# Performance work log

Hardware: AMD Instinct MI355X
Metric: run time of the kernel (lower is better)

## Reference

```python
import jax, jax.numpy as jnp
import numpy as np

# dims
B, S, E, H, W = 32, 256, 512, 512, 512   # batch, max_sentence_length, word_emb, rnn_units, weight_size
ENC = 2 * H                               # bidirectional encoder hidden
V = 50000                                 # vocab


def setup_inputs() -> dict:
    key = jax.random.key(0)
    ks = jax.random.split(key, 16)
    n = jax.random.normal
    return {
        "word_ids": jax.random.randint(ks[0], (B, S), 0, V),
        "encoder_outputs": n(ks[1], (B, S, ENC), jnp.float32),
        "encoder_hn": n(ks[2], (B, H), jnp.float32),          # initial decoder cell state
        "emb": n(ks[3], (V, E), jnp.float32) * 0.02,          # WordFeature embedding table
        "chunk_emb": n(ks[4], (S, W), jnp.float32) * 0.02,    # chunk_length_embedding
        "W1": n(ks[5], (ENC, W), jnp.float32) / np.sqrt(ENC),
        "W2": n(ks[6], (E, W), jnp.float32) / np.sqrt(E),
        "W3": n(ks[7], (E, W), jnp.float32) / np.sqrt(E),
        "W4": n(ks[8], (H, W), jnp.float32) / np.sqrt(H),
        "vt1": n(ks[9], (W,), jnp.float32) / np.sqrt(W),
        "vt2": n(ks[10], (W,), jnp.float32) / np.sqrt(W),
        "Wx": n(ks[11], (E, 4 * H), jnp.float32) / np.sqrt(E),  # decoder LSTM cell
        "Wh": n(ks[12], (H, 4 * H), jnp.float32) / np.sqrt(H),
        "bias": jnp.zeros((4 * H,), jnp.float32),
    }


def reference(word_ids, encoder_outputs, encoder_hn, emb, chunk_emb,
              W1, W2, W3, W4, vt1, vt2, Wx, Wh, bias):
    Ss = word_ids.shape[1]
    Hh = encoder_hn.shape[1]
    inp = emb[word_ids]                                   # [B,S,E] word features
    b1 = jnp.einsum('bse,ew->bsw', encoder_outputs, W1)   # W1(encoder_output), hoisted
    b2 = jnp.einsum('bse,ew->bsw', inp, W2)               # W2(single_input), hoisted
    pos = jnp.arange(Ss)

    def decode_one(inp_b, b1_b, b2_b, c0):
        def step(carry, _):
            last_bond, bond, h, c, out_vec = carry
            done = bond >= Ss
            # decoder input: mean of current segment inp[last_bond:bond] (zeros at step 0)
            m = ((pos >= last_bond) & (pos < bond)).astype(inp_b.dtype)  # [S]
            x = (m @ inp_b) / jnp.maximum(m.sum(), 1.0)                  # [E]
            # LSTM cell (stand-in for decoder.pointer_forward)
            gates = x @ Wx + h @ Wh + bias                               # [4H]
            i_g, f_g, g_g, o_g = jnp.split(gates, 4)
            c_n = jax.nn.sigmoid(f_g) * c + jax.nn.sigmoid(i_g) * jnp.tanh(g_g)
            h_n = jax.nn.sigmoid(o_g) * jnp.tanh(c_n)
            h2 = jnp.where(done, h, h_n)
            c2 = jnp.where(done, c, c_n)
            bidx = jnp.minimum(bond, Ss - 1)
            # pointer attention over positions >= bond
            blend = jnp.tanh(b1_b + b2_b + inp_b[bidx] @ W3 + h2 @ W4)   # [S,W]
            seg_len = jnp.clip(bond - last_bond, 0, Ss - 1)
            scores = blend @ vt1 + chunk_emb[seg_len] @ vt2              # [S]
            scores = jnp.where(pos >= bidx, scores, -1e30)
            # log_softmax is monotonic -> argmax of scores == argmax of log-probs
            idx = jnp.argmax(scores)                                     # absolute = max_index + bond
            new_bond = jnp.where(idx > bond, idx, bond + 1)              # force progress
            widx = jnp.minimum(new_bond, Ss - 1)
            val = jnp.where((~done) & (new_bond < Ss), 1.0, out_vec[widx])
            out_new = out_vec.at[widx].set(val)
            last2 = jnp.where(done, last_bond, bond)
            bond2 = jnp.where(done, bond, new_bond)
            return (last2, bond2, h2, c2, out_new), None

        init = (jnp.int32(0), jnp.int32(0),
                jnp.zeros((Hh,), inp_b.dtype), c0,
                jnp.zeros((Ss,), inp_b.dtype))
        (_, _, _, _, out_vec), _ = jax.lax.scan(step, init, None, length=Ss)
        return out_vec

    outs = jax.vmap(decode_one)(inp, b1, b2, encoder_hn)   # [B,S]
    return outs.T                                          # [S,B] == torch.stack(output_list, 1)
```

## Files before the change

### kernel.cpp

```cpp
#include <hip/hip_runtime.h>
#include <math.h>

#define Bn   32
#define Sn   256
#define En   512
#define Hn   512
#define Wn   512
#define ENCn 1024
#define G4   2048
#define KTOT 1536
#define NC   8
#define WPC  32

#define OFF_BSUM  0L
#define OFF_U3    4194304L
#define OFF_PE    8388608L
#define OFF_WB    12599296L
#define OFF_W4B   14696448L
#define OFF_GATES 14958592L
#define OFF_H     15089664L
#define OFF_C     15106048L
#define OFF_SPART 15138816L
#define OFF_STATE 15204352L


__device__ __forceinline__ float aload(const float* p) {
    return __hip_atomic_load(p, __ATOMIC_RELAXED, __HIP_MEMORY_SCOPE_AGENT);
}
__device__ __forceinline__ void astore(float* p, float v) {
    __hip_atomic_store(p, v, __ATOMIC_RELAXED, __HIP_MEMORY_SCOPE_AGENT);
}
__device__ __forceinline__ int aiload(const int* p) {
    return __hip_atomic_load(p, __ATOMIC_RELAXED, __HIP_MEMORY_SCOPE_AGENT);
}
__device__ __forceinline__ void aistore(int* p, int v) {
    __hip_atomic_store(p, v, __ATOMIC_RELAXED, __HIP_MEMORY_SCOPE_AGENT);
}

__global__ void init_kernel(const float* __restrict__ hn0, float* __restrict__ h,
                            float* __restrict__ c, int* __restrict__ state)
{
    int i = blockIdx.x * blockDim.x + threadIdx.x;
    if (i < Bn * Hn) { h[i] = 0.0f; c[i] = hn0[i]; }
    if (i < 8192) state[i] = (i == 64) ? Bn : 0;
}

__global__ void wtrans_kernel(const float* __restrict__ Wx, const float* __restrict__ Wh,
                              const float* __restrict__ W4, float* __restrict__ WB,
                              float* __restrict__ W4B)
{
    int idx = blockIdx.x * 256 + threadIdx.x;
    if (idx < 2097152) {
        const int cc = idx & 3, l = (idx >> 2) & 63, kq = (idx >> 8) & 255, cb = idx >> 16;
        const int k = 4 * kq + cc, j = cb * 64 + l;
        WB[idx] = (k < 512) ? Wx[(long)k * G4 + j] : Wh[(long)(k - 512) * G4 + j];
    }
    if (idx < 262144) {
        const int cc = idx & 3, l = (idx >> 2) & 63, kq = (idx >> 8) & 127, cb = idx >> 15;
        const int k = 4 * kq + cc, j = cb * 64 + l;
        W4B[idx] = W4[(long)k * Wn + j];
    }
}

__global__ void pe1_kernel(const int* __restrict__ wid, const float* __restrict__ emb,
                           float* __restrict__ pb)
{
    const int b = blockIdx.x, blk = blockIdx.y;
    __shared__ int wids[16];
    if (threadIdx.x < 16) wids[threadIdx.x] = wid[b * Sn + blk * 16 + threadIdx.x];
    __syncthreads();
    float a0 = 0.f, a1 = 0.f;
    for (int s = 0; s < 16; ++s) {
        const float* r = emb + (long)wids[s] * En;
        a0 += r[threadIdx.x]; a1 += r[threadIdx.x + 256];
    }
    pb[((long)b * 16 + blk) * En + threadIdx.x] = a0;
    pb[((long)b * 16 + blk) * En + threadIdx.x + 256] = a1;
}

__global__ void pe2_kernel(const int* __restrict__ wid, const float* __restrict__ emb,
                           const float* __restrict__ pb, float* __restrict__ pe)
{
    const int b = blockIdx.x, blk = blockIdx.y;
    __shared__ int wids[16];
    if (threadIdx.x < 16) wids[threadIdx.x] = wid[b * Sn + blk * 16 + threadIdx.x];
    __syncthreads();
    float a0 = 0.f, a1 = 0.f;
    for (int j = 0; j < blk; ++j) {
        a0 += pb[((long)b * 16 + j) * En + threadIdx.x];
        a1 += pb[((long)b * 16 + j) * En + threadIdx.x + 256];
    }
    float* base = pe + (long)b * 257 * En;
    if (blk == 0) { base[threadIdx.x] = 0.f; base[threadIdx.x + 256] = 0.f; }
    for (int s = 0; s < 16; ++s) {
        const float* r = emb + (long)wids[s] * En;
        a0 += r[threadIdx.x]; a1 += r[threadIdx.x + 256];
        float* o = base + (long)(blk * 16 + s + 1) * En;
        o[threadIdx.x] = a0; o[threadIdx.x + 256] = a1;
    }
}

__global__ __launch_bounds__(256) void bsum_gemm(
    const float* __restrict__ enc, const int* __restrict__ wid,
    const float* __restrict__ emb, const float* __restrict__ W1,
    const float* __restrict__ W2, float* __restrict__ bsum)
{
    __shared__ float As[16][68];
    __shared__ float Bs[16][68];
    const int tid  = threadIdx.x;
    const int row0 = blockIdx.y * 64;
    const int col0 = blockIdx.x * 64;
    const int tm0  = (tid & 15) * 4;
    const int tn0  = (tid >> 4) * 4;
    const int la_r = tid >> 2;
    const int la_k = (tid & 3) * 4;
    const int lb_k = tid >> 4;
    const int lb_n = (tid & 15) * 4;

    float acc[4][4];
#pragma unroll
    for (int i = 0; i < 4; i++)
#pragma unroll
        for (int j = 0; j < 4; j++) acc[i][j] = 0.0f;

    for (int k0 = 0; k0 < KTOT; k0 += 16) {
        const int gr = row0 + la_r;
        float4 av;
        if (k0 < ENCn) {
            av = *(const float4*)&enc[(long)gr * ENCn + k0 + la_k];
        } else {
            const int wv = wid[gr];
            av = *(const float4*)&emb[(long)wv * En + (k0 - ENCn) + la_k];
        }
        As[la_k + 0][la_r] = av.x;
        As[la_k + 1][la_r] = av.y;
        As[la_k + 2][la_r] = av.z;
        As[la_k + 3][la_r] = av.w;
        float4 bv;
        if (k0 < ENCn) bv = *(const float4*)&W1[(long)(k0 + lb_k) * Wn + col0 + lb_n];
        else           bv = *(const float4*)&W2[(long)(k0 - ENCn + lb_k) * Wn + col0 + lb_n];
        *(float4*)&Bs[lb_k][lb_n] = bv;
        __syncthreads();
#pragma unroll
        for (int kk = 0; kk < 16; kk++) {
            float4 a = *(const float4*)&As[kk][tm0];
            float4 b = *(const float4*)&Bs[kk][tn0];
            acc[0][0] += a.x * b.x; acc[0][1] += a.x * b.y; acc[0][2] += a.x * b.z; acc[0][3] += a.x * b.w;
            acc[1][0] += a.y * b.x; acc[1][1] += a.y * b.y; acc[1][2] += a.y * b.z; acc[1][3] += a.y * b.w;
            acc[2][0] += a.z * b.x; acc[2][1] += a.z * b.y; acc[2][2] += a.z * b.z; acc[2][3] += a.z * b.w;
            acc[3][0] += a.w * b.x; acc[3][1] += a.w * b.y; acc[3][2] += a.w * b.z; acc[3][3] += a.w * b.w;
        }
        __syncthreads();
    }
#pragma unroll
    for (int i = 0; i < 4; i++) {
        float4 o = make_float4(acc[i][0], acc[i][1], acc[i][2], acc[i][3]);
        *(float4*)&bsum[(long)(row0 + tm0 + i) * Wn + col0 + tn0] = o;
    }
}

__global__ __launch_bounds__(256) void u3_gemm(
    const int* __restrict__ wid, const float* __restrict__ emb,
    const float* __restrict__ W3, float* __restrict__ u3)
{
    __shared__ float As[16][68];
    __shared__ float Bs[16][68];
    const int tid  = threadIdx.x;
    const int row0 = blockIdx.y * 64;
    const int col0 = blockIdx.x * 64;
    const int tm0  = (tid & 15) * 4;
    const int tn0  = (tid >> 4) * 4;
    const int la_r = tid >> 2;
    const int la_k = (tid & 3) * 4;
    const int lb_k = tid >> 4;
    const int lb_n = (tid & 15) * 4;

    float acc[4][4];
#pragma unroll
    for (int i = 0; i < 4; i++)
#pragma unroll
        for (int j = 0; j < 4; j++) acc[i][j] = 0.0f;

    for (int k0 = 0; k0 < 512; k0 += 16) {
        const int gr = row0 + la_r;
        const int wv = wid[gr];
        float4 av = *(const float4*)&emb[(long)wv * En + k0 + la_k];
        As[la_k + 0][la_r] = av.x;
        As[la_k + 1][la_r] = av.y;
        As[la_k + 2][la_r] = av.z;
        As[la_k + 3][la_r] = av.w;
        *(float4*)&Bs[lb_k][lb_n] = *(const float4*)&W3[(long)(k0 + lb_k) * Wn + col0 + lb_n];
        __syncthreads();
#pragma unroll
        for (int kk = 0; kk < 16; kk++) {
            float4 a = *(const float4*)&As[kk][tm0];
            float4 b = *(const float4*)&Bs[kk][tn0];
            acc[0][0] += a.x * b.x; acc[0][1] += a.x * b.y; acc[0][2] += a.x * b.z; acc[0][3] += a.x * b.w;
            acc[1][0] += a.y * b.x; acc[1][1] += a.y * b.y; acc[1][2] += a.y * b.z; acc[1][3] += a.y * b.w;
            acc[2][0] += a.z * b.x; acc[2][1] += a.z * b.y; acc[2][2] += a.z * b.z; acc[2][3] += a.z * b.w;
            acc[3][0] += a.w * b.x; acc[3][1] += a.w * b.y; acc[3][2] += a.w * b.z; acc[3][3] += a.w * b.w;
        }
        __syncthreads();
    }
#pragma unroll
    for (int i = 0; i < 4; i++) {
        float4 o = make_float4(acc[i][0], acc[i][1], acc[i][2], acc[i][3]);
        *(float4*)&u3[(long)(row0 + tm0 + i) * Wn + col0 + tn0] = o;
    }
}

__device__ __forceinline__ int gbar(int* st, const int* nact, int wg, int round)
{
    __shared__ int s_done;
    __syncthreads();
    if (threadIdx.x == 0) {
        const int c = wg >> 5;
        int* lc = st + 4096 + 256 * c;
        int* lr = lc + 64;
        int flag = 0;
        bool wait = true;
        int a = __hip_atomic_fetch_add(lc, 1, __ATOMIC_RELAXED, __HIP_MEMORY_SCOPE_AGENT);
        if (a == round * WPC - 1) {
            int g = __hip_atomic_fetch_add(st + 80, 1, __ATOMIC_RELAXED, __HIP_MEMORY_SCOPE_AGENT);
            if (g == round * NC - 1) {
                const int d = (aiload(nact) == 0) ? (1 << 30) : 0;
                flag = round | d;
                for (int k = 0; k < NC; ++k)
                    aistore(st + 4096 + 256 * k + 64, flag);
                wait = false;
            }
        }
        if (wait) {
            for (;;) {
                flag = aiload(lr);
                if ((flag & 0x3FFFFFFF) >= round) break;
                __builtin_amdgcn_s_sleep(1);
            }
        }
        s_done = (flag >> 30) & 1;
    }
    __syncthreads();
    return s_done;
}

__global__ __launch_bounds__(256) void decode_kernel(
    const float* __restrict__ bias, const float* __restrict__ vt1,
    const float* __restrict__ bsum, const float* __restrict__ u3,
    const float* __restrict__ pe,   const float* __restrict__ WB,
    const float* __restrict__ W4B,  float* __restrict__ gpart,
    float* __restrict__ hbuf, float* __restrict__ cbuf,
    float* __restrict__ spart,
    int* __restrict__ state, float* __restrict__ out)
{
    __shared__ __align__(16) float wlds[32768];
    __shared__ __align__(16) float sx[4096];
    __shared__ __align__(16) float sred[2048];
    __shared__ float s_svt[64];
    __shared__ float s_wv[4];
    __shared__ int   s_wi[4];
    __shared__ int   s_last;
    __shared__ int   s_bd[8], s_ls[8];

    const int wg   = blockIdx.x;
    const int tid  = threadIdx.x;
    const int lane = tid & 63;
    const int wv   = tid >> 6;

    int* bond = state;
    int* last = state + 32;
    int* nact = state + 64;

    const int cb1 = wg & 31;
    const int kh  = (wg >> 5) & 1;
    const int bg  = wg >> 6;
    const int b2  = wg >> 3;
    const int cb2 = wg & 7;
    const float4* W4B4 = (const float4*)W4B;
    float4* wlds4 = (float4*)wlds;
    float4* sx4   = (float4*)sx;

    {
        const float4* src = (const float4*)WB + ((long)cb1 * 256 + kh * 128) * 64;
        for (int i = tid; i < 8192; i += 256) wlds4[i] = src[i];
    }
    if (tid < 64) s_svt[tid] = vt1[cb2 * 64 + tid];

    int myround = 0;

    for (int step = 0; step < Sn; ++step) {
        const float* cold = cbuf + (step & 1) * (Bn * Hn);
        float*       cnew = cbuf + ((step + 1) & 1) * (Bn * Hn);

        if (tid < 8) {
            s_bd[tid] = aiload(&bond[bg * 8 + tid]);
            s_ls[tid] = aiload(&last[bg * 8 + tid]);
        }
        __syncthreads();
        for (int idx = tid; idx < 4096; idx += 256) {
            const int bq = idx >> 9, k = idx & 511;
            const int b  = bg * 8 + bq;
            float v;
            if (kh == 0) {
                const int bd = s_bd[bq], ls = s_ls[bq];
                const float inv = 1.0f / (float)max(bd - ls, 1);
                v = (pe[((long)b * 257 + bd) * En + k] - pe[((long)b * 257 + ls) * En + k]) * inv;
            } else {
                v = aload(&hbuf[b * Hn + k]);
            }
            sx[idx] = v;
        }
        __syncthreads();
        {
            float acc[8] = {0.f,0.f,0.f,0.f,0.f,0.f,0.f,0.f};
            const float4* wl = wlds4 + (wv * 32) * 64 + lane;
#pragma unroll 8
            for (int kq = 0; kq < 32; ++kq) {
                const float4 w = wl[kq * 64];
                const int kb = wv * 32 + kq;
#pragma unroll
                for (int bq = 0; bq < 8; ++bq) {
                    const float4 xv = sx4[bq * 128 + kb];
                    acc[bq] += w.x * xv.x + w.y * xv.y + w.z * xv.z + w.w * xv.w;
                }
            }
#pragma unroll
            for (int bq = 0; bq < 8; ++bq)
                sred[wv * 512 + bq * 64 + lane] = acc[bq];
        }
        __syncthreads();
#pragma unroll
        for (int o = tid; o < 512; o += 256) {
            const int bq = o >> 6;
            if (s_bd[bq] < Sn) {
                const float s = sred[o] + sred[512 + o] + sred[1024 + o] + sred[1536 + o];
                astore(&gpart[((long)(kh * Bn) + bg * 8 + bq) * G4 + cb1 * 64 + (o & 63)], s);
            }
        }
        gbar(state, nact, wg, 2 * step + 1);

        const int bd = aiload(&bond[b2]);
        if (bd < Sn) {
            ++myround;
            const float* gp0 = gpart + (long)b2 * G4;
            const float* gp1 = gpart + (long)(Bn + b2) * G4;
            for (int j = tid; j < Hn; j += 256) {
                const float ig = aload(&gp0[j])        + aload(&gp1[j])        + bias[j];
                const float fg = aload(&gp0[512 + j])  + aload(&gp1[512 + j])  + bias[512 + j];
                const float gg = aload(&gp0[1024 + j]) + aload(&gp1[1024 + j]) + bias[1024 + j];
                const float og = aload(&gp0[1536 + j]) + aload(&gp1[1536 + j]) + bias[1536 + j];
                const float co = aload(&cold[b2 * Hn + j]);
                const float sf  = 1.f / (1.f + expf(-fg));
                const float sig = 1.f / (1.f + expf(-ig));
                const float so  = 1.f / (1.f + expf(-og));
                const float cn  = sf * co + sig * tanhf(gg);
                const float h2  = so * tanhf(cn);
                sx[j] = h2;
                if (cb2 == 0) { astore(&hbuf[b2 * Hn + j], h2); astore(&cnew[b2 * Hn + j], cn); }
            }
            __syncthreads();
            {
                float acc = 0.f;
                const float4* wrow = W4B4 + ((long)cb2 * 128 + wv * 32) * 64 + lane;
#pragma unroll 8
                for (int kq = 0; kq < 32; ++kq) {
                    const float4 w  = wrow[(long)kq * 64];
                    const float4 xv = sx4[wv * 32 + kq];
                    acc += w.x * xv.x + w.y * xv.y + w.z * xv.z + w.w * xv.w;
                }
                sx[512 + wv * 64 + lane] = acc;
            }
            __syncthreads();
            if (tid < 64) {
                const float* u3row = u3 + ((long)b2 * Sn + bd) * Wn + cb2 * 64;
                sx[768 + tid] = sx[512 + tid] + sx[576 + tid] + sx[640 + tid]
                              + sx[704 + tid] + u3row[tid];
            }
            __syncthreads();
            if (tid >= bd) {
                const float* row = bsum + ((long)b2 * Sn + tid) * Wn + cb2 * 64;
                float a = 0.f;
#pragma unroll 8
                for (int i = 0; i < 64; ++i)
                    a += tanhf(row[i] + sx[768 + i]) * s_svt[i];
                astore(&spart[((long)b2 * 8 + cb2) * 256 + tid], a);
            }
            __syncthreads();
            if (tid == 0) {
                int o = __hip_atomic_fetch_add(state + 256 + 64 * b2, 1,
                                               __ATOMIC_RELAXED, __HIP_MEMORY_SCOPE_AGENT);
                s_last = (o == myround * 8 - 1);
            }
            __syncthreads();
            if (s_last) {
                float v = -3.402823e38f; int vi = Sn;
                if (tid >= bd) {
                    const float* sp = spart + (long)b2 * 8 * 256 + tid;
                    float s = 0.f;
#pragma unroll
                    for (int k = 0; k < 8; ++k) s += aload(&sp[k * 256]);
                    v = s; vi = tid;
                }
#pragma unroll
                for (int off = 32; off; off >>= 1) {
                    const float v2 = __shfl_xor(v, off, 64);
                    const int   i2 = __shfl_xor(vi, off, 64);
                    if (v2 > v || (v2 == v && i2 < vi)) { v = v2; vi = i2; }
                }
                if (lane == 0) { s_wv[wv] = v; s_wi[wv] = vi; }
                __syncthreads();
                if (tid == 0) {
                    float bv = s_wv[0]; int bi = s_wi[0];
#pragma unroll
                    for (int k = 1; k < 4; ++k)
                        if (s_wv[k] > bv || (s_wv[k] == bv && s_wi[k] < bi)) { bv = s_wv[k]; bi = s_wi[k]; }
                    const int nb2 = (bi > bd) ? bi : bd + 1;
                    if (nb2 < Sn) out[nb2 * Bn + b2] = 1.0f;
                    else __hip_atomic_fetch_add(nact, -1, __ATOMIC_RELAXED, __HIP_MEMORY_SCOPE_AGENT);
                    aistore(&last[b2], bd);
                    aistore(&bond[b2], nb2);
                }
            }
        }
        if (gbar(state, nact, wg, 2 * step + 2)) break;
    }
}

extern "C" void kernel_launch(void* const* d_in, const int* in_sizes, int n_in,
                              void* d_out, int out_size, void* d_ws, size_t ws_size,
                              hipStream_t stream)
{
    const int*   wid  = (const int*)d_in[0];
    const float* enc  = (const float*)d_in[1];
    const float* hn0  = (const float*)d_in[2];
    const float* emb  = (const float*)d_in[3];
    const float* W1   = (const float*)d_in[5];
    const float* W2   = (const float*)d_in[6];
    const float* W3   = (const float*)d_in[7];
    const float* W4   = (const float*)d_in[8];
    const float* vt1  = (const float*)d_in[9];
    const float* Wx   = (const float*)d_in[11];
    const float* Wh   = (const float*)d_in[12];
    const float* bias = (const float*)d_in[13];

    float* ws    = (float*)d_ws;
    float* bsum  = ws + OFF_BSUM;
    float* u3    = ws + OFF_U3;
    float* pb    = ws + OFF_U3;
    float* pe    = ws + OFF_PE;
    float* WB    = ws + OFF_WB;
    float* W4B   = ws + OFF_W4B;
    float* gpart = ws + OFF_GATES;
    float* h     = ws + OFF_H;
    float* c     = ws + OFF_C;
    float* spart = ws + OFF_SPART;
    int*   state = (int*)(ws + OFF_STATE);
    float* out   = (float*)d_out;

    hipMemsetAsync(d_out, 0, (size_t)Sn * Bn * sizeof(float), stream);
    hipLaunchKernelGGL(init_kernel, dim3(64), dim3(256), 0, stream, hn0, h, c, state);
    hipLaunchKernelGGL(wtrans_kernel, dim3(8192), dim3(256), 0, stream, Wx, Wh, W4, WB, W4B);
    hipLaunchKernelGGL(pe1_kernel, dim3(32, 16), dim3(256), 0, stream, wid, emb, pb);
    hipLaunchKernelGGL(pe2_kernel, dim3(32, 16), dim3(256), 0, stream, wid, emb, pb, pe);
    hipLaunchKernelGGL(u3_gemm, dim3(8, 128), dim3(256), 0, stream, wid, emb, W3, u3);
    hipLaunchKernelGGL(bsum_gemm, dim3(8, 128), dim3(256), 0, stream, enc, wid, emb, W1, W2, bsum);

    void* args[] = { (void*)&bias, (void*)&vt1, (void*)&bsum, (void*)&u3, (void*)&pe,
                     (void*)&WB, (void*)&W4B, (void*)&gpart, (void*)&h, (void*)&c,
                     (void*)&spart, (void*)&state, (void*)&out };
    hipLaunchCooperativeKernel((void*)decode_kernel, dim3(256), dim3(256), args, 0, stream);
}
```

Baseline: 923.5 us.

## Replace global grid barriers with per-batch counters and packed state flags

```diff
diff --git a/kernel.cpp b/kernel.cpp
--- a/kernel.cpp
+++ b/kernel.cpp
@@ -9,8 +9,6 @@
 #define ENCn 1024
 #define G4   2048
 #define KTOT 1536
-#define NC   8
-#define WPC  32
 
 #define OFF_BSUM  0L
 #define OFF_U3    4194304L
@@ -33,7 +31,10 @@
 __device__ __forceinline__ int aiload(const int* p) {
     return __hip_atomic_load(p, __ATOMIC_RELAXED, __HIP_MEMORY_SCOPE_AGENT);
 }
-__device__ __forceinline__ void aistore(int* p, int v) {
+__device__ __forceinline__ unsigned long long aload64(const unsigned long long* p) {
+    return __hip_atomic_load(p, __ATOMIC_RELAXED, __HIP_MEMORY_SCOPE_AGENT);
+}
+__device__ __forceinline__ void astore64(unsigned long long* p, unsigned long long v) {
     __hip_atomic_store(p, v, __ATOMIC_RELAXED, __HIP_MEMORY_SCOPE_AGENT);
 }
 
@@ -42,7 +43,7 @@
 {
     int i = blockIdx.x * blockDim.x + threadIdx.x;
     if (i < Bn * Hn) { h[i] = 0.0f; c[i] = hn0[i]; }
-    if (i < 8192) state[i] = (i == 64) ? Bn : 0;
+    if (i < 8192) state[i] = (i == 1024) ? Bn : 0;
 }
 
 __global__ void wtrans_kernel(const float* __restrict__ Wx, const float* __restrict__ Wh,
@@ -209,40 +210,6 @@
     }
 }
 
-__device__ __forceinline__ int gbar(int* st, const int* nact, int wg, int round)
-{
-    __shared__ int s_done;
-    __syncthreads();
-    if (threadIdx.x == 0) {
-        const int c = wg >> 5;
-        int* lc = st + 4096 + 256 * c;
-        int* lr = lc + 64;
-        int flag = 0;
-        bool wait = true;
-        int a = __hip_atomic_fetch_add(lc, 1, __ATOMIC_RELAXED, __HIP_MEMORY_SCOPE_AGENT);
-        if (a == round * WPC - 1) {
-            int g = __hip_atomic_fetch_add(st + 80, 1, __ATOMIC_RELAXED, __HIP_MEMORY_SCOPE_AGENT);
-            if (g == round * NC - 1) {
-                const int d = (aiload(nact) == 0) ? (1 << 30) : 0;
-                flag = round | d;
-                for (int k = 0; k < NC; ++k)
-                    aistore(st + 4096 + 256 * k + 64, flag);
-                wait = false;
-            }
-        }
-        if (wait) {
-            for (;;) {
-                flag = aiload(lr);
-                if ((flag & 0x3FFFFFFF) >= round) break;
-                __builtin_amdgcn_s_sleep(1);
-            }
-        }
-        s_done = (flag >> 30) & 1;
-    }
-    __syncthreads();
-    return s_done;
-}
-
 __global__ __launch_bounds__(256) void decode_kernel(
     const float* __restrict__ bias, const float* __restrict__ vt1,
     const float* __restrict__ bsum, const float* __restrict__ u3,
@@ -260,21 +227,24 @@
     __shared__ int   s_wi[4];
     __shared__ int   s_last;
     __shared__ int   s_bd[8], s_ls[8];
+    __shared__ int   s_exit;
 
     const int wg   = blockIdx.x;
     const int tid  = threadIdx.x;
     const int lane = tid & 63;
     const int wv   = tid >> 6;
 
-    int* bond = state;
-    int* last = state + 32;
-    int* nact = state + 64;
+    int* gcnt = state;
+    int* scnt = state + 512;
+    int* nact = state + 1024;
+    unsigned long long* s64b = (unsigned long long*)(state + 1536);
 
     const int cb1 = wg & 31;
     const int kh  = (wg >> 5) & 1;
     const int bg  = wg >> 6;
     const int b2  = wg >> 3;
     const int cb2 = wg & 7;
+    const int bq2 = (wg >> 3) & 7;
     const float4* W4B4 = (const float4*)W4B;
     float4* wlds4 = (float4*)wlds;
     float4* sx4   = (float4*)sx;
@@ -285,62 +255,94 @@
     }
     if (tid < 64) s_svt[tid] = vt1[cb2 * 64 + tid];
 
-    int myround = 0;
-
-    for (int step = 0; step < Sn; ++step) {
-        const float* cold = cbuf + (step & 1) * (Bn * Hn);
-        float*       cnew = cbuf + ((step + 1) & 1) * (Bn * Hn);
-
-        if (tid < 8) {
-            s_bd[tid] = aiload(&bond[bg * 8 + tid]);
-            s_ls[tid] = aiload(&last[bg * 8 + tid]);
+    int a_b = 0;
+
+    for (int t = 1; t <= Sn; ++t) {
+        if (tid < 64) {
+            const bool isb = tid < 8;
+            const unsigned long long* sp = s64b + 8 * (bg * 8 + (tid & 7));
+            for (;;) {
+                unsigned long long pk = isb ? aload64(sp) : 0ULL;
+                const int ep = (int)(pk & 0xffffu);
+                const int bd = (int)((pk >> 16) & 0xffffu);
+                const bool ok = !isb || (ep >= t - 1) || (bd >= Sn);
+                int ex = 0;
+                if (tid == 8) ex = (aiload(nact) == 0);
+                const unsigned long long bal  = __ballot(ok);
+                const unsigned long long balx = __ballot(ex != 0);
+                if (((bal & 0xffULL) == 0xffULL) || balx) {
+                    if (isb) { s_bd[tid] = bd; s_ls[tid] = (int)((pk >> 32) & 0xffffu); }
+                    if (tid == 0) s_exit = (balx != 0ULL);
+                    break;
+                }
+                __builtin_amdgcn_s_sleep(1);
+            }
         }
         __syncthreads();
-        for (int idx = tid; idx < 4096; idx += 256) {
-            const int bq = idx >> 9, k = idx & 511;
-            const int b  = bg * 8 + bq;
-            float v;
-            if (kh == 0) {
-                const int bd = s_bd[bq], ls = s_ls[bq];
-                const float inv = 1.0f / (float)max(bd - ls, 1);
-                v = (pe[((long)b * 257 + bd) * En + k] - pe[((long)b * 257 + ls) * En + k]) * inv;
-            } else {
-                v = aload(&hbuf[b * Hn + k]);
-            }
-            sx[idx] = v;
-        }
-        __syncthreads();
-        {
-            float acc[8] = {0.f,0.f,0.f,0.f,0.f,0.f,0.f,0.f};
-            const float4* wl = wlds4 + (wv * 32) * 64 + lane;
+        if (s_exit) break;
+
+        int anyact = 0;
+#pragma unroll
+        for (int q = 0; q < 8; ++q) anyact |= (s_bd[q] < Sn);
+
+        if (anyact) {
+            for (int idx = tid; idx < 4096; idx += 256) {
+                const int bq = idx >> 9, k = idx & 511;
+                const int b  = bg * 8 + bq;
+                float v = 0.f;
+                if (s_bd[bq] < Sn) {
+                    if (kh == 0) {
+                        const int bd = s_bd[bq], ls = s_ls[bq];
+                        const float inv = 1.0f / (float)max(bd - ls, 1);
+                        v = (pe[((long)b * 257 + bd) * En + k] - pe[((long)b * 257 + ls) * En + k]) * inv;
+                    } else {
+                        v = aload(&hbuf[b * Hn + k]);
+                    }
+                }
+                sx[idx] = v;
+            }
+            __syncthreads();
+            {
+                float acc[8] = {0.f,0.f,0.f,0.f,0.f,0.f,0.f,0.f};
+                const float4* wl = wlds4 + (wv * 32) * 64 + lane;
 #pragma unroll 8
-            for (int kq = 0; kq < 32; ++kq) {
-                const float4 w = wl[kq * 64];
-                const int kb = wv * 32 + kq;
-#pragma unroll
-                for (int bq = 0; bq < 8; ++bq) {
-                    const float4 xv = sx4[bq * 128 + kb];
-                    acc[bq] += w.x * xv.x + w.y * xv.y + w.z * xv.z + w.w * xv.w;
-                }
-            }
-#pragma unroll
-            for (int bq = 0; bq < 8; ++bq)
-                sred[wv * 512 + bq * 64 + lane] = acc[bq];
-        }
-        __syncthreads();
-#pragma unroll
-        for (int o = tid; o < 512; o += 256) {
-            const int bq = o >> 6;
-            if (s_bd[bq] < Sn) {
-                const float s = sred[o] + sred[512 + o] + sred[1024 + o] + sred[1536 + o];
-                astore(&gpart[((long)(kh * Bn) + bg * 8 + bq) * G4 + cb1 * 64 + (o & 63)], s);
-            }
-        }
-        gbar(state, nact, wg, 2 * step + 1);
-
-        const int bd = aiload(&bond[b2]);
+                for (int kq = 0; kq < 32; ++kq) {
+                    const float4 w = wl[kq * 64];
+                    const int kb = wv * 32 + kq;
+#pragma unroll
+                    for (int bq = 0; bq < 8; ++bq) {
+                        const float4 xv = sx4[bq * 128 + kb];
+                        acc[bq] += w.x * xv.x + w.y * xv.y + w.z * xv.z + w.w * xv.w;
+                    }
+                }
+#pragma unroll
+                for (int bq = 0; bq < 8; ++bq)
+                    sred[wv * 512 + bq * 64 + lane] = acc[bq];
+            }
+            __syncthreads();
+#pragma unroll
+            for (int o = tid; o < 512; o += 256) {
+                const int bq = o >> 6;
+                if (s_bd[bq] < Sn) {
+                    const float s = sred[o] + sred[512 + o] + sred[1024 + o] + sred[1536 + o];
+                    astore(&gpart[((long)(kh * Bn) + bg * 8 + bq) * G4 + cb1 * 64 + (o & 63)], s);
+                }
+            }
+            __syncthreads();
+        }
+        if (tid < 8)
+            __hip_atomic_fetch_add(&gcnt[16 * (bg * 8 + tid)], 1,
+                                   __ATOMIC_RELAXED, __HIP_MEMORY_SCOPE_AGENT);
+
+        const int bd = s_bd[bq2];
         if (bd < Sn) {
-            ++myround;
+            ++a_b;
+            const float* cold = cbuf + ((a_b - 1) & 1) * (Bn * Hn);
+            float*       cnew = cbuf + (a_b & 1) * (Bn * Hn);
+            if (tid == 0) {
+                while (aiload(&gcnt[16 * b2]) < 64 * t) __builtin_amdgcn_s_sleep(1);
+            }
+            __syncthreads();
             const float* gp0 = gpart + (long)b2 * G4;
             const float* gp1 = gpart + (long)(Bn + b2) * G4;
             for (int j = tid; j < Hn; j += 256) {
@@ -386,9 +388,9 @@
             }
             __syncthreads();
             if (tid == 0) {
-                int o = __hip_atomic_fetch_add(state + 256 + 64 * b2, 1,
+                int o = __hip_atomic_fetch_add(&scnt[16 * b2], 1,
                                                __ATOMIC_RELAXED, __HIP_MEMORY_SCOPE_AGENT);
-                s_last = (o == myround * 8 - 1);
+                s_last = (o == 8 * a_b - 1);
             }
             __syncthreads();
             if (s_last) {
@@ -416,12 +418,14 @@
                     const int nb2 = (bi > bd) ? bi : bd + 1;
                     if (nb2 < Sn) out[nb2 * Bn + b2] = 1.0f;
                     else __hip_atomic_fetch_add(nact, -1, __ATOMIC_RELAXED, __HIP_MEMORY_SCOPE_AGENT);
-                    aistore(&last[b2], bd);
-                    aistore(&bond[b2], nb2);
-                }
-            }
-        }
-        if (gbar(state, nact, wg, 2 * step + 2)) break;
+                    const unsigned long long pk =
+                        (unsigned long long)(unsigned)t |
+                        ((unsigned long long)(unsigned)nb2 << 16) |
+                        ((unsigned long long)(unsigned)bd  << 32);
+                    astore64(&s64b[8 * b2], pk);
+                }
+            }
+        }
     }
 }
 
```

Result: faster. 865.7 us (-6.3%).

## Precompute prefix-sum input projection and replace global barriers with per-batch flags

Applied to the files above, without the earlier changes.

```diff
diff --git a/kernel.cpp b/kernel.cpp
--- a/kernel.cpp
+++ b/kernel.cpp
@@ -9,20 +9,18 @@
 #define ENCn 1024
 #define G4   2048
 #define KTOT 1536
-#define NC   8
-#define WPC  32
 
 #define OFF_BSUM  0L
-#define OFF_U3    4194304L
-#define OFF_PE    8388608L
-#define OFF_WB    12599296L
-#define OFF_W4B   14696448L
-#define OFF_GATES 14958592L
-#define OFF_H     15089664L
-#define OFF_C     15106048L
-#define OFF_SPART 15138816L
-#define OFF_STATE 15204352L
-
+#define OFF_PWX   4194304L
+#define OFF_PE    21037056L
+#define OFF_U3    21037056L
+#define OFF_WHB   25247744L
+#define OFF_W4B   26296320L
+#define OFF_GPH   26558464L
+#define OFF_SPART 26689536L
+#define OFF_STATE 26820608L
+
+typedef unsigned long long u64t;
 
 __device__ __forceinline__ float aload(const float* p) {
     return __hip_atomic_load(p, __ATOMIC_RELAXED, __HIP_MEMORY_SCOPE_AGENT);
@@ -36,24 +34,32 @@
 __device__ __forceinline__ void aistore(int* p, int v) {
     __hip_atomic_store(p, v, __ATOMIC_RELAXED, __HIP_MEMORY_SCOPE_AGENT);
 }
-
-__global__ void init_kernel(const float* __restrict__ hn0, float* __restrict__ h,
-                            float* __restrict__ c, int* __restrict__ state)
+__device__ __forceinline__ u64t aload64(const u64t* p) {
+    return __hip_atomic_load(p, __ATOMIC_RELAXED, __HIP_MEMORY_SCOPE_AGENT);
+}
+__device__ __forceinline__ void astore64(u64t* p, u64t v) {
+    __hip_atomic_store(p, v, __ATOMIC_RELAXED, __HIP_MEMORY_SCOPE_AGENT);
+}
+__device__ __forceinline__ u64t pack2(float a, float b) {
+    return (u64t)__float_as_uint(a) | ((u64t)__float_as_uint(b) << 32);
+}
+__device__ __forceinline__ float lo32(u64t v) { return __uint_as_float((unsigned)(v & 0xffffffffu)); }
+__device__ __forceinline__ float hi32(u64t v) { return __uint_as_float((unsigned)(v >> 32)); }
+
+__global__ void init_kernel(float* __restrict__ gph, int* __restrict__ state)
 {
     int i = blockIdx.x * blockDim.x + threadIdx.x;
-    if (i < Bn * Hn) { h[i] = 0.0f; c[i] = hn0[i]; }
-    if (i < 8192) state[i] = (i == 64) ? Bn : 0;
-}
-
-__global__ void wtrans_kernel(const float* __restrict__ Wx, const float* __restrict__ Wh,
-                              const float* __restrict__ W4, float* __restrict__ WB,
-                              float* __restrict__ W4B)
+    if (i < 131072) gph[i] = 0.0f;
+    if (i < 8192) state[i] = (i < 512) ? 1 : 0;
+}
+
+__global__ void wtrans_kernel(const float* __restrict__ Wh, const float* __restrict__ W4,
+                              float* __restrict__ WhB, float* __restrict__ W4B)
 {
     int idx = blockIdx.x * 256 + threadIdx.x;
-    if (idx < 2097152) {
-        const int cc = idx & 3, l = (idx >> 2) & 63, kq = (idx >> 8) & 255, cb = idx >> 16;
-        const int k = 4 * kq + cc, j = cb * 64 + l;
-        WB[idx] = (k < 512) ? Wx[(long)k * G4 + j] : Wh[(long)(k - 512) * G4 + j];
+    if (idx < 1048576) {
+        const int c = idx & 255, k = (idx >> 8) & 511, cb = idx >> 17;
+        WhB[idx] = Wh[(long)k * G4 + cb * 256 + c];
     }
     if (idx < 262144) {
         const int cc = idx & 3, l = (idx >> 2) & 63, kq = (idx >> 8) & 127, cb = idx >> 15;
@@ -159,9 +165,8 @@
     }
 }
 
-__global__ __launch_bounds__(256) void u3_gemm(
-    const int* __restrict__ wid, const float* __restrict__ emb,
-    const float* __restrict__ W3, float* __restrict__ u3)
+__global__ __launch_bounds__(256) void swx_gemm(
+    const float* __restrict__ pe, const float* __restrict__ Wx, float* __restrict__ PWX)
 {
     __shared__ float As[16][68];
     __shared__ float Bs[16][68];
@@ -182,6 +187,58 @@
         for (int j = 0; j < 4; j++) acc[i][j] = 0.0f;
 
     for (int k0 = 0; k0 < 512; k0 += 16) {
+        int gr = row0 + la_r; if (gr > 8223) gr = 8223;
+        float4 av = *(const float4*)&pe[(long)gr * En + k0 + la_k];
+        As[la_k + 0][la_r] = av.x;
+        As[la_k + 1][la_r] = av.y;
+        As[la_k + 2][la_r] = av.z;
+        As[la_k + 3][la_r] = av.w;
+        *(float4*)&Bs[lb_k][lb_n] = *(const float4*)&Wx[(long)(k0 + lb_k) * G4 + col0 + lb_n];
+        __syncthreads();
+#pragma unroll
+        for (int kk = 0; kk < 16; kk++) {
+            float4 a = *(const float4*)&As[kk][tm0];
+            float4 b = *(const float4*)&Bs[kk][tn0];
+            acc[0][0] += a.x * b.x; acc[0][1] += a.x * b.y; acc[0][2] += a.x * b.z; acc[0][3] += a.x * b.w;
+            acc[1][0] += a.y * b.x; acc[1][1] += a.y * b.y; acc[1][2] += a.y * b.z; acc[1][3] += a.y * b.w;
+            acc[2][0] += a.z * b.x; acc[2][1] += a.z * b.y; acc[2][2] += a.z * b.z; acc[2][3] += a.z * b.w;
+            acc[3][0] += a.w * b.x; acc[3][1] += a.w * b.y; acc[3][2] += a.w * b.z; acc[3][3] += a.w * b.w;
+        }
+        __syncthreads();
+    }
+#pragma unroll
+    for (int i = 0; i < 4; i++) {
+        const int r = row0 + tm0 + i;
+        if (r < 8224) {
+            float4 o = make_float4(acc[i][0], acc[i][1], acc[i][2], acc[i][3]);
+            *(float4*)&PWX[(long)r * G4 + col0 + tn0] = o;
+        }
+    }
+}
+
+__global__ __launch_bounds__(256) void u3_gemm(
+    const int* __restrict__ wid, const float* __restrict__ emb,
+    const float* __restrict__ W3, float* __restrict__ u3)
+{
+    __shared__ float As[16][68];
+    __shared__ float Bs[16][68];
+    const int tid  = threadIdx.x;
+    const int row0 = blockIdx.y * 64;
+    const int col0 = blockIdx.x * 64;
+    const int tm0  = (tid & 15) * 4;
+    const int tn0  = (tid >> 4) * 4;
+    const int la_r = tid >> 2;
+    const int la_k = (tid & 3) * 4;
+    const int lb_k = tid >> 4;
+    const int lb_n = (tid & 15) * 4;
+
+    float acc[4][4];
+#pragma unroll
+    for (int i = 0; i < 4; i++)
+#pragma unroll
+        for (int j = 0; j < 4; j++) acc[i][j] = 0.0f;
+
+    for (int k0 = 0; k0 < 512; k0 += 16) {
         const int gr = row0 + la_r;
         const int wv = wid[gr];
         float4 av = *(const float4*)&emb[(long)wv * En + k0 + la_k];
@@ -209,219 +266,190 @@
     }
 }
 
-__device__ __forceinline__ int gbar(int* st, const int* nact, int wg, int round)
-{
-    __shared__ int s_done;
-    __syncthreads();
-    if (threadIdx.x == 0) {
-        const int c = wg >> 5;
-        int* lc = st + 4096 + 256 * c;
-        int* lr = lc + 64;
-        int flag = 0;
-        bool wait = true;
-        int a = __hip_atomic_fetch_add(lc, 1, __ATOMIC_RELAXED, __HIP_MEMORY_SCOPE_AGENT);
-        if (a == round * WPC - 1) {
-            int g = __hip_atomic_fetch_add(st + 80, 1, __ATOMIC_RELAXED, __HIP_MEMORY_SCOPE_AGENT);
-            if (g == round * NC - 1) {
-                const int d = (aiload(nact) == 0) ? (1 << 30) : 0;
-                flag = round | d;
-                for (int k = 0; k < NC; ++k)
-                    aistore(st + 4096 + 256 * k + 64, flag);
-                wait = false;
-            }
-        }
-        if (wait) {
-            for (;;) {
-                flag = aiload(lr);
-                if ((flag & 0x3FFFFFFF) >= round) break;
-                __builtin_amdgcn_s_sleep(1);
-            }
-        }
-        s_done = (flag >> 30) & 1;
-    }
-    __syncthreads();
-    return s_done;
-}
-
 __global__ __launch_bounds__(256) void decode_kernel(
     const float* __restrict__ bias, const float* __restrict__ vt1,
     const float* __restrict__ bsum, const float* __restrict__ u3,
-    const float* __restrict__ pe,   const float* __restrict__ WB,
-    const float* __restrict__ W4B,  float* __restrict__ gpart,
-    float* __restrict__ hbuf, float* __restrict__ cbuf,
-    float* __restrict__ spart,
-    int* __restrict__ state, float* __restrict__ out)
+    const float* __restrict__ PWX,  const float* __restrict__ WhB,
+    const float* __restrict__ W4B,  float* __restrict__ gphbuf,
+    float* __restrict__ spart, int* __restrict__ state,
+    const float* __restrict__ hn0, float* __restrict__ out)
 {
     __shared__ __align__(16) float wlds[32768];
-    __shared__ __align__(16) float sx[4096];
-    __shared__ __align__(16) float sred[2048];
+    __shared__ __align__(16) float pwx[2][2048];
+    __shared__ __align__(16) float hld[512];
+    __shared__ __align__(16) float cld[512];
+    __shared__ __align__(16) float sgph[4][256];
+    __shared__ __align__(16) float sred4[4][64];
+    __shared__ float qv[64];
     __shared__ float s_svt[64];
     __shared__ float s_wv[4];
     __shared__ int   s_wi[4];
-    __shared__ int   s_last;
-    __shared__ int   s_bd[8], s_ls[8];
 
     const int wg   = blockIdx.x;
     const int tid  = threadIdx.x;
     const int lane = tid & 63;
     const int wv   = tid >> 6;
-
-    int* bond = state;
-    int* last = state + 32;
-    int* nact = state + 64;
-
-    const int cb1 = wg & 31;
-    const int kh  = (wg >> 5) & 1;
-    const int bg  = wg >> 6;
-    const int b2  = wg >> 3;
-    const int cb2 = wg & 7;
+    const int b    = wg >> 3;
+    const int cb2  = wg & 7;
+
+    int* gflag = state;
+    int* sflag = state + 512;
+    u64t* gph64 = (u64t*)gphbuf;
     const float4* W4B4 = (const float4*)W4B;
     float4* wlds4 = (float4*)wlds;
-    float4* sx4   = (float4*)sx;
+    const float4* h4 = (const float4*)hld;
 
     {
-        const float4* src = (const float4*)WB + ((long)cb1 * 256 + kh * 128) * 64;
+        const float4* src = W4B4 + (long)cb2 * 8192;
         for (int i = tid; i < 8192; i += 256) wlds4[i] = src[i];
     }
     if (tid < 64) s_svt[tid] = vt1[cb2 * 64 + tid];
-
-    int myround = 0;
-
-    for (int step = 0; step < Sn; ++step) {
-        const float* cold = cbuf + (step & 1) * (Bn * Hn);
-        float*       cnew = cbuf + ((step + 1) & 1) * (Bn * Hn);
+    cld[tid]       = hn0[b * Hn + tid];
+    cld[256 + tid] = hn0[b * Hn + 256 + tid];
+    hld[tid] = 0.f; hld[256 + tid] = 0.f;
+    {
+        const float4* pr = (const float4*)(PWX + (long)b * 257 * G4);
+        float4* d = (float4*)pwx[0];
+        for (int i = tid; i < 512; i += 256) d[i] = pr[i];
+    }
+    const float2* bias2 = (const float2*)bias;
+    const float2 bi  = bias2[tid];
+    const float2 bf  = bias2[256 + tid];
+    const float2 bg_ = bias2[512 + tid];
+    const float2 bo  = bias2[768 + tid];
+    __syncthreads();
+
+    int bd = 0, ls = 0;
+
+    for (int t = 1; t <= Sn; ++t) {
+        const int cur = t & 1, prv = cur ^ 1;
 
         if (tid < 8) {
-            s_bd[tid] = aiload(&bond[bg * 8 + tid]);
-            s_ls[tid] = aiload(&last[bg * 8 + tid]);
-        }
-        __syncthreads();
-        for (int idx = tid; idx < 4096; idx += 256) {
-            const int bq = idx >> 9, k = idx & 511;
-            const int b  = bg * 8 + bq;
-            float v;
-            if (kh == 0) {
-                const int bd = s_bd[bq], ls = s_ls[bq];
-                const float inv = 1.0f / (float)max(bd - ls, 1);
-                v = (pe[((long)b * 257 + bd) * En + k] - pe[((long)b * 257 + ls) * En + k]) * inv;
-            } else {
-                v = aload(&hbuf[b * Hn + k]);
-            }
-            sx[idx] = v;
+            const int* g = gflag + 16 * b + tid;
+            while (aiload(g) < t) __builtin_amdgcn_s_sleep(1);
         }
         __syncthreads();
         {
-            float acc[8] = {0.f,0.f,0.f,0.f,0.f,0.f,0.f,0.f};
-            const float4* wl = wlds4 + (wv * 32) * 64 + lane;
+            const float4* pr = (const float4*)(PWX + ((long)b * 257 + bd) * G4);
+            float4* d = (float4*)pwx[cur];
+            for (int i = tid; i < 512; i += 256) d[i] = pr[i];
+        }
+        float u3v = 0.f;
+        if (tid < 64) u3v = aload(&u3[((long)b * Sn + bd) * Wn + cb2 * 64 + tid]);
+        const long gb = (long)cur * 32768 + (long)b * 1024;
+        const u64t g0 = aload64(&gph64[gb + tid]);
+        const u64t g1 = aload64(&gph64[gb + 256 + tid]);
+        const u64t g2 = aload64(&gph64[gb + 512 + tid]);
+        const u64t g3 = aload64(&gph64[gb + 768 + tid]);
+        __syncthreads();
+
+        {
+            const float inv = 1.0f / (float)max(bd - ls, 1);
+            const int j0 = 2 * tid, j1 = j0 + 1;
+            const float igA = (pwx[cur][j0]        - pwx[prv][j0])        * inv + lo32(g0) + bi.x;
+            const float igB = (pwx[cur][j1]        - pwx[prv][j1])        * inv + hi32(g0) + bi.y;
+            const float fgA = (pwx[cur][512 + j0]  - pwx[prv][512 + j0])  * inv + lo32(g1) + bf.x;
+            const float fgB = (pwx[cur][512 + j1]  - pwx[prv][512 + j1])  * inv + hi32(g1) + bf.y;
+            const float ggA = (pwx[cur][1024 + j0] - pwx[prv][1024 + j0]) * inv + lo32(g2) + bg_.x;
+            const float ggB = (pwx[cur][1024 + j1] - pwx[prv][1024 + j1]) * inv + hi32(g2) + bg_.y;
+            const float ogA = (pwx[cur][1536 + j0] - pwx[prv][1536 + j0]) * inv + lo32(g3) + bo.x;
+            const float ogB = (pwx[cur][1536 + j1] - pwx[prv][1536 + j1]) * inv + hi32(g3) + bo.y;
+            const float sfA = 1.f / (1.f + expf(-fgA));
+            const float siA = 1.f / (1.f + expf(-igA));
+            const float soA = 1.f / (1.f + expf(-ogA));
+            const float cnA = sfA * cld[j0] + siA * tanhf(ggA);
+            const float h2A = soA * tanhf(cnA);
+            const float sfB = 1.f / (1.f + expf(-fgB));
+            const float siB = 1.f / (1.f + expf(-igB));
+            const float soB = 1.f / (1.f + expf(-ogB));
+            const float cnB = sfB * cld[j1] + siB * tanhf(ggB);
+            const float h2B = soB * tanhf(cnB);
+            cld[j0] = cnA; hld[j0] = h2A;
+            cld[j1] = cnB; hld[j1] = h2B;
+        }
+        __syncthreads();
+
+        {
+            float acc = 0.f;
+            const float4* wr = wlds4 + (wv * 32) * 64 + lane;
 #pragma unroll 8
             for (int kq = 0; kq < 32; ++kq) {
-                const float4 w = wl[kq * 64];
-                const int kb = wv * 32 + kq;
-#pragma unroll
-                for (int bq = 0; bq < 8; ++bq) {
-                    const float4 xv = sx4[bq * 128 + kb];
-                    acc[bq] += w.x * xv.x + w.y * xv.y + w.z * xv.z + w.w * xv.w;
-                }
+                const float4 w = wr[kq * 64];
+                const float4 hv = h4[wv * 32 + kq];
+                acc += w.x * hv.x + w.y * hv.y + w.z * hv.z + w.w * hv.w;
             }
-#pragma unroll
-            for (int bq = 0; bq < 8; ++bq)
-                sred[wv * 512 + bq * 64 + lane] = acc[bq];
-        }
-        __syncthreads();
-#pragma unroll
-        for (int o = tid; o < 512; o += 256) {
-            const int bq = o >> 6;
-            if (s_bd[bq] < Sn) {
-                const float s = sred[o] + sred[512 + o] + sred[1024 + o] + sred[1536 + o];
-                astore(&gpart[((long)(kh * Bn) + bg * 8 + bq) * G4 + cb1 * 64 + (o & 63)], s);
+            sred4[wv][lane] = acc;
+        }
+        __syncthreads();
+        if (tid < 64) qv[tid] = sred4[0][tid] + sred4[1][tid] + sred4[2][tid] + sred4[3][tid] + u3v;
+        __syncthreads();
+
+        if (tid >= bd) {
+            const float* row = bsum + ((long)b * Sn + tid) * Wn + cb2 * 64;
+            float a = 0.f;
+#pragma unroll 8
+            for (int i = 0; i < 64; ++i)
+                a += tanhf(row[i] + qv[i]) * s_svt[i];
+            astore(&spart[(long)cur * 65536 + (long)b * 2048 + cb2 * 256 + tid], a);
+        }
+
+        {
+            float4 acc = make_float4(0.f, 0.f, 0.f, 0.f);
+            const float* wb = WhB + (long)cb2 * 131072;
+            const int k0 = wv * 128;
+#pragma unroll 4
+            for (int k = k0; k < k0 + 128; ++k) {
+                const float hk = hld[k];
+                const float4 w = *(const float4*)&wb[(long)k * 256 + lane * 4];
+                acc.x += hk * w.x; acc.y += hk * w.y; acc.z += hk * w.z; acc.w += hk * w.w;
             }
-        }
-        gbar(state, nact, wg, 2 * step + 1);
-
-        const int bd = aiload(&bond[b2]);
-        if (bd < Sn) {
-            ++myround;
-            const float* gp0 = gpart + (long)b2 * G4;
-            const float* gp1 = gpart + (long)(Bn + b2) * G4;
-            for (int j = tid; j < Hn; j += 256) {
-                const float ig = aload(&gp0[j])        + aload(&gp1[j])        + bias[j];
-                const float fg = aload(&gp0[512 + j])  + aload(&gp1[512 + j])  + bias[512 + j];
-                const float gg = aload(&gp0[1024 + j]) + aload(&gp1[1024 + j]) + bias[1024 + j];
-                const float og = aload(&gp0[1536 + j]) + aload(&gp1[1536 + j]) + bias[1536 + j];
-                const float co = aload(&cold[b2 * Hn + j]);
-                const float sf  = 1.f / (1.f + expf(-fg));
-                const float sig = 1.f / (1.f + expf(-ig));
-                const float so  = 1.f / (1.f + expf(-og));
-                const float cn  = sf * co + sig * tanhf(gg);
-                const float h2  = so * tanhf(cn);
-                sx[j] = h2;
-                if (cb2 == 0) { astore(&hbuf[b2 * Hn + j], h2); astore(&cnew[b2 * Hn + j], cn); }
-            }
-            __syncthreads();
-            {
-                float acc = 0.f;
-                const float4* wrow = W4B4 + ((long)cb2 * 128 + wv * 32) * 64 + lane;
-#pragma unroll 8
-                for (int kq = 0; kq < 32; ++kq) {
-                    const float4 w  = wrow[(long)kq * 64];
-                    const float4 xv = sx4[wv * 32 + kq];
-                    acc += w.x * xv.x + w.y * xv.y + w.z * xv.z + w.w * xv.w;
-                }
-                sx[512 + wv * 64 + lane] = acc;
-            }
-            __syncthreads();
-            if (tid < 64) {
-                const float* u3row = u3 + ((long)b2 * Sn + bd) * Wn + cb2 * 64;
-                sx[768 + tid] = sx[512 + tid] + sx[576 + tid] + sx[640 + tid]
-                              + sx[704 + tid] + u3row[tid];
-            }
-            __syncthreads();
-            if (tid >= bd) {
-                const float* row = bsum + ((long)b2 * Sn + tid) * Wn + cb2 * 64;
-                float a = 0.f;
-#pragma unroll 8
-                for (int i = 0; i < 64; ++i)
-                    a += tanhf(row[i] + sx[768 + i]) * s_svt[i];
-                astore(&spart[((long)b2 * 8 + cb2) * 256 + tid], a);
-            }
-            __syncthreads();
-            if (tid == 0) {
-                int o = __hip_atomic_fetch_add(state + 256 + 64 * b2, 1,
-                                               __ATOMIC_RELAXED, __HIP_MEMORY_SCOPE_AGENT);
-                s_last = (o == myround * 8 - 1);
-            }
-            __syncthreads();
-            if (s_last) {
-                float v = -3.402823e38f; int vi = Sn;
-                if (tid >= bd) {
-                    const float* sp = spart + (long)b2 * 8 * 256 + tid;
-                    float s = 0.f;
-#pragma unroll
-                    for (int k = 0; k < 8; ++k) s += aload(&sp[k * 256]);
-                    v = s; vi = tid;
-                }
-#pragma unroll
-                for (int off = 32; off; off >>= 1) {
-                    const float v2 = __shfl_xor(v, off, 64);
-                    const int   i2 = __shfl_xor(vi, off, 64);
-                    if (v2 > v || (v2 == v && i2 < vi)) { v = v2; vi = i2; }
-                }
-                if (lane == 0) { s_wv[wv] = v; s_wi[wv] = vi; }
-                __syncthreads();
-                if (tid == 0) {
-                    float bv = s_wv[0]; int bi = s_wi[0];
-#pragma unroll
-                    for (int k = 1; k < 4; ++k)
-                        if (s_wv[k] > bv || (s_wv[k] == bv && s_wi[k] < bi)) { bv = s_wv[k]; bi = s_wi[k]; }
-                    const int nb2 = (bi > bd) ? bi : bd + 1;
-                    if (nb2 < Sn) out[nb2 * Bn + b2] = 1.0f;
-                    else __hip_atomic_fetch_add(nact, -1, __ATOMIC_RELAXED, __HIP_MEMORY_SCOPE_AGENT);
-                    aistore(&last[b2], bd);
-                    aistore(&bond[b2], nb2);
-                }
-            }
-        }
-        if (gbar(state, nact, wg, 2 * step + 2)) break;
+            *(float4*)&sgph[wv][lane * 4] = acc;
+        }
+        __syncthreads();
+        if (tid < 128) {
+            const int c0 = 2 * tid, c1 = c0 + 1;
+            const float lo = sgph[0][c0] + sgph[1][c0] + sgph[2][c0] + sgph[3][c0];
+            const float hi = sgph[0][c1] + sgph[1][c1] + sgph[2][c1] + sgph[3][c1];
+            astore64(&gph64[(long)prv * 32768 + (long)b * 1024 + cb2 * 128 + tid], pack2(lo, hi));
+        }
+        __syncthreads();
+
+        if (tid == 0) {
+            aistore(&sflag[16 * b + cb2], t);
+            aistore(&gflag[16 * b + cb2], t + 1);
+        }
+        if (tid < 8) {
+            const int* s = sflag + 16 * b + tid;
+            while (aiload(s) < t) __builtin_amdgcn_s_sleep(1);
+        }
+        __syncthreads();
+        float v = -3.402823e38f; int vi = Sn;
+        if (tid >= bd) {
+            const float* sp = spart + (long)cur * 65536 + (long)b * 2048 + tid;
+            float s = 0.f;
+#pragma unroll
+            for (int k = 0; k < 8; ++k) s += aload(&sp[k * 256]);
+            v = s; vi = tid;
+        }
+#pragma unroll
+        for (int off = 32; off; off >>= 1) {
+            const float v2 = __shfl_xor(v, off, 64);
+            const int   i2 = __shfl_xor(vi, off, 64);
+            if (v2 > v || (v2 == v && i2 < vi)) { v = v2; vi = i2; }
+        }
+        if (lane == 0) { s_wv[wv] = v; s_wi[wv] = vi; }
+        __syncthreads();
+        {
+            float bv = s_wv[0]; int bi_ = s_wi[0];
+#pragma unroll
+            for (int k = 1; k < 4; ++k)
+                if (s_wv[k] > bv || (s_wv[k] == bv && s_wi[k] < bi_)) { bv = s_wv[k]; bi_ = s_wi[k]; }
+            const int nb = (bi_ > bd) ? bi_ : bd + 1;
+            if (cb2 == 0 && tid == 0 && nb < Sn) out[nb * Bn + b] = 1.0f;
+            ls = bd; bd = nb;
+        }
+        __syncthreads();
+        if (bd >= Sn) break;
     }
 }
 
@@ -444,28 +472,30 @@
 
     float* ws    = (float*)d_ws;
     float* bsum  = ws + OFF_BSUM;
+    float* PWX   = ws + OFF_PWX;
+    float* pe    = ws + OFF_PE;
+    float* pb    = ws + OFF_WHB;
     float* u3    = ws + OFF_U3;
-    float* pb    = ws + OFF_U3;
-    float* pe    = ws + OFF_PE;
-    float* WB    = ws + OFF_WB;
+    float* WhB   = ws + OFF_WHB;
     float* W4B   = ws + OFF_W4B;
-    float* gpart = ws + OFF_GATES;
-    float* h     = ws + OFF_H;
-    float* c     = ws + OFF_C;
+    float* gph   = ws + OFF_GPH;
     float* spart = ws + OFF_SPART;
     int*   state = (int*)(ws + OFF_STATE);
     float* out   = (float*)d_out;
 
-    hipMemsetAsync(d_out, 0, (size_t)Sn * Bn * sizeof(float), stream);
-    hipLaunchKernelGGL(init_kernel, dim3(64), dim3(256), 0, stream, hn0, h, c, state);
-    hipLaunchKernelGGL(wtrans_kernel, dim3(8192), dim3(256), 0, stream, Wx, Wh, W4, WB, W4B);
+    pb = ws + OFF_BSUM;
+
+    (void)hipMemsetAsync(d_out, 0, (size_t)Sn * Bn * sizeof(float), stream);
+    hipLaunchKernelGGL(init_kernel, dim3(544), dim3(256), 0, stream, gph, state);
+    hipLaunchKernelGGL(wtrans_kernel, dim3(4096), dim3(256), 0, stream, Wh, W4, WhB, W4B);
     hipLaunchKernelGGL(pe1_kernel, dim3(32, 16), dim3(256), 0, stream, wid, emb, pb);
     hipLaunchKernelGGL(pe2_kernel, dim3(32, 16), dim3(256), 0, stream, wid, emb, pb, pe);
+    hipLaunchKernelGGL(swx_gemm, dim3(32, 129), dim3(256), 0, stream, pe, Wx, PWX);
     hipLaunchKernelGGL(u3_gemm, dim3(8, 128), dim3(256), 0, stream, wid, emb, W3, u3);
     hipLaunchKernelGGL(bsum_gemm, dim3(8, 128), dim3(256), 0, stream, enc, wid, emb, W1, W2, bsum);
 
-    void* args[] = { (void*)&bias, (void*)&vt1, (void*)&bsum, (void*)&u3, (void*)&pe,
-                     (void*)&WB, (void*)&W4B, (void*)&gpart, (void*)&h, (void*)&c,
-                     (void*)&spart, (void*)&state, (void*)&out };
-    hipLaunchCooperativeKernel((void*)decode_kernel, dim3(256), dim3(256), args, 0, stream);
-}
+    void* args[] = { (void*)&bias, (void*)&vt1, (void*)&bsum, (void*)&u3, (void*)&PWX,
+                     (void*)&WhB, (void*)&W4B, (void*)&gph, (void*)&spart,
+                     (void*)&state, (void*)&hn0, (void*)&out };
+    (void)hipLaunchCooperativeKernel((void*)decode_kernel, dim3(256), dim3(256), args, 0, stream);
+}
```

After: 940.7 us. About the same (+1.9%).
